# Kernel tuning notes

Measured on AMD Instinct MI355X. Metric: run time of the kernel, lower is better.

Reference implementation:

```python
import jax, jax.numpy as jnp
import numpy as np

B, S, D = 2, 2048, 2048
H, KVH = 16, 4
HD = D // H  # 128


def _rope_angles(seq, head_dim):
    theta = 1.0 / (10000.0 ** (jnp.arange(0, head_dim, 2, dtype=jnp.float32) / head_dim))
    ang = jnp.arange(seq, dtype=jnp.float32)[:, None] * theta[None, :]  # [S, HD/2]
    return jnp.cos(ang), jnp.sin(ang)


def _apply_rotary(t, cos, sin):
    # t: [B, S, h, HD]; pairs are (even, odd) along last dim (view_as_complex semantics)
    tr = t[..., 0::2]
    ti = t[..., 1::2]
    c = cos[None, :, None, :]
    s = sin[None, :, None, :]
    out_r = tr * c - ti * s
    out_i = tr * s + ti * c
    return jnp.stack([out_r, out_i], axis=-1).reshape(t.shape)


def setup_inputs() -> dict:
    key = jax.random.key(0)
    ks = jax.random.split(key, 8)
    sd = 1.0 / np.sqrt(D)
    return {
        'x': jax.random.normal(ks[0], (B, S, D), dtype=jnp.float32),
        'wq': jax.random.normal(ks[1], (D, D), dtype=jnp.float32) * sd,
        'bq': jax.random.normal(ks[2], (D,), dtype=jnp.float32) * 0.01,
        'wk': jax.random.normal(ks[3], (D, KVH * HD), dtype=jnp.float32) * sd,
        'bk': jax.random.normal(ks[4], (KVH * HD,), dtype=jnp.float32) * 0.01,
        'wv': jax.random.normal(ks[5], (D, KVH * HD), dtype=jnp.float32) * sd,
        'bv': jax.random.normal(ks[6], (KVH * HD,), dtype=jnp.float32) * 0.01,
        'wo': jax.random.normal(ks[7], (D, D), dtype=jnp.float32) * sd,
    }


def reference(x, wq, bq, wk, bk, wv, bv, wo):
    b, s, d = x.shape
    q = (x @ wq + bq).reshape(b, s, H, HD)
    k = (x @ wk + bk).reshape(b, s, KVH, HD)
    v = (x @ wv + bv).reshape(b, s, KVH, HD)

    cos, sin = _rope_angles(s, HD)
    q = _apply_rotary(q, cos, sin)
    k = _apply_rotary(k, cos, sin)

    repeat = H // KVH
    k = jnp.repeat(k, repeat, axis=2)  # [B, S, H, HD]
    v = jnp.repeat(v, repeat, axis=2)

    scale = 1.0 / np.sqrt(HD)
    att_score = jnp.einsum('bqhd,bkhd->bqhk', q, k) * scale  # [B, S, H, S]
    att_weight = jax.nn.softmax(att_score, axis=-1)
    out = jnp.einsum('bqhk,bkhd->bqhd', att_weight, v)
    out = out.reshape(b, s, H * HD)
    return out @ wo
```

## Files before the change

### kernel.cpp

```cpp
#include <hip/hip_runtime.h>
#include <hip/hip_bf16.h>
#include <cstdint>

typedef __attribute__((ext_vector_type(4))) float f32x4;
typedef __attribute__((ext_vector_type(16))) float f32x16;
typedef __attribute__((ext_vector_type(8))) short bf16x8;
typedef __attribute__((ext_vector_type(4))) unsigned int u32x4;
typedef unsigned short u16;
typedef unsigned int u32;

__device__ __forceinline__ u16 f2b(float x) {
  __hip_bfloat16 h = __float2bfloat16(x);
  return *reinterpret_cast<u16*>(&h);
}

__device__ __forceinline__ float b2f(u32 u) {
  u32 v = u << 16;
  return __builtin_bit_cast(float, v);
}

__device__ __forceinline__ u32 pk(float a, float b) {
  __hip_bfloat162 h2 = __float22bfloat162_rn(float2{a, b});
  return *reinterpret_cast<u32*>(&h2);
}

__device__ __forceinline__ void gload16(const void* g, void* l) {
  __builtin_amdgcn_global_load_lds((const __attribute__((address_space(1))) u32*)g,
                                   (__attribute__((address_space(3))) u32*)l, 16, 0, 0);
}

__device__ __forceinline__ float xmax32(float x) {
  return fmaxf(x, __shfl_xor(x, 32, 64));
}
__device__ __forceinline__ float xsum32(float x) {
  return x + __shfl_xor(x, 32, 64);
}


__global__ void cvt_f32_bf16(const float* __restrict__ in, u16* __restrict__ out, int n4) {
  int idx = (blockIdx.x * 256 + threadIdx.x);
  if (idx < n4) {
    const float4 v = *(const float4*)(in + (size_t)idx * 4);
    u16* o = out + (size_t)idx * 4;
    o[0] = f2b(v.x); o[1] = f2b(v.y); o[2] = f2b(v.z); o[3] = f2b(v.w);
  }
}

__global__ void w_transpose_cvt(const float* __restrict__ w0, const float* __restrict__ w1,
                                const float* __restrict__ w2, int b0, int b1,
                                int N0, int N1, int N2,
                                u16* __restrict__ out, int K) {
  __shared__ float tile[32][33];
  int k0 = blockIdx.x * 32, n0 = blockIdx.y * 32;
  const float* src; int srcN; int c0;
  if (n0 < b0)      { src = w0; srcN = N0; c0 = n0; }
  else if (n0 < b1) { src = w1; srcN = N1; c0 = n0 - b0; }
  else              { src = w2; srcN = N2; c0 = n0 - b1; }
  int tx = threadIdx.x & 31, ty = threadIdx.x >> 5;
#pragma unroll
  for (int j = 0; j < 32; j += 8)
    tile[ty + j][tx] = src[(size_t)(k0 + ty + j) * srcN + c0 + tx];
  __syncthreads();
#pragma unroll
  for (int j = 0; j < 32; j += 8)
    out[(size_t)(n0 + ty + j) * K + k0 + tx] = f2b(tile[tx][ty + j]);
}

__global__ void pack_bias(const float* __restrict__ bq, const float* __restrict__ bk,
                          const float* __restrict__ bv, float* __restrict__ out) {
  int i = blockIdx.x * 256 + threadIdx.x;
  if (i < 3072) out[i] = (i < 2048) ? bq[i] : ((i < 2560) ? bk[i - 2048] : bv[i - 2560]);
}

__global__ void v_transpose_cvt(const u16* __restrict__ qkv, u16* __restrict__ vt) {
  __shared__ u16 tile[32][34];
  int s0 = blockIdx.x * 32;
  int d0 = blockIdx.y * 32;
  int z = blockIdx.z;
  int b = z >> 2, kvh = z & 3;
  int tx = threadIdx.x & 31, ty = threadIdx.x >> 5;
#pragma unroll
  for (int j = 0; j < 32; j += 8)
    tile[ty + j][tx] = qkv[((size_t)(b * 2048 + s0 + ty + j)) * 3072 + 2560 + kvh * 128 + d0 + tx];
  __syncthreads();
#pragma unroll
  for (int j = 0; j < 32; j += 8)
    vt[((size_t)z * 128 + d0 + ty + j) * 2048 + s0 + tx] = tile[tx][ty + j];
}

__global__ void rope_cvt(const u16* __restrict__ qkv, u16* __restrict__ out,
                         int lognh, int col0, float scale) {
  int idx = blockIdx.x * 256 + threadIdx.x;
  int i = idx & 63;
  int nh = 1 << lognh;
  int h = (idx >> 6) & (nh - 1);
  int bs = idx >> (6 + lognh);
  int s = bs & 2047;
  int b = bs >> 11;
  u32 pr = *(const u32*)(qkv + (size_t)bs * 3072 + col0 + h * 128 + 2 * i);
  float tr = b2f(pr & 0xffffu), ti = b2f(pr >> 16);
  float theta = expf(-(float)i * 0.14391156831212787f);
  float ang = (float)s * theta;
  float sv, cv;
  sincosf(ang, &sv, &cv);
  float orr = (tr * cv - ti * sv) * scale;
  float oii = (tr * sv + ti * cv) * scale;
  *(u32*)(out + (((size_t)(b * nh + h) * 2048 + s) * 128 + 2 * i)) = pk(orr, oii);
}

__global__ __launch_bounds__(512, 2) void gemm256_bt(
    const u16* __restrict__ A, const u16* __restrict__ Bt,
    const float* __restrict__ bias, void* __restrict__ Cv,
    int M, int N, int K, int gx, int obf16) {
  __shared__ u16 lds[65536];
  const int tid = threadIdx.x, lane = tid & 63;
  const int w = tid >> 6, wr = w >> 2, wc = w & 3;
  const int nb = gridDim.x;
  const int swz = (blockIdx.x & 7) * (nb >> 3) + (blockIdx.x >> 3);
  const int m0 = (swz / gx) * 256, n0 = (swz % gx) * 256;
  const int l15 = lane & 15;
  const int gx16 = ((lane >> 4) * 16) ^ (((l15 >> 1) & 3) << 4);

#define GL(X, kh, bufi, t)                                                      \
  { _Pragma("unroll")                                                           \
    for (int rd = 0; rd < 2; ++rd) {                                            \
      int c = tid + rd * 512;                                                   \
      int row = c >> 2;                                                         \
      int sx = ((c & 3) * 16) ^ (((row >> 1) & 3) << 4);                        \
      const u16* srcp = ((X) ? Bt + (size_t)(n0 + row) * K                      \
                             : A + (size_t)(m0 + row) * K) + (t) * 64 + (kh) * 32; \
      gload16((const char*)srcp + sx,                                           \
              (char*)lds + (bufi) * 65536 + (X) * 32768 + (kh) * 16384 + c * 16); \
    } }

  f32x4 acc[8][4] = {};
  const int NT = K >> 6;

  GL(0, 0, 0, 0) GL(1, 0, 0, 0) GL(0, 1, 0, 0) GL(1, 1, 0, 0)

  for (int t = 0; t < NT; ++t) {
    const int buf = t & 1, nbuf = buf ^ 1;
    const int tn = (t + 1 < NT) ? t + 1 : NT - 1;
    const char* Ab = (const char*)lds + buf * 65536;
    const char* Bb = Ab + 32768;
    bf16x8 af[4], bfr[4];

    asm volatile("s_waitcnt vmcnt(4)" ::: "memory");
    __builtin_amdgcn_s_barrier();
    GL(0, 0, nbuf, tn)
#pragma unroll
    for (int n = 0; n < 4; ++n)
      bfr[n] = *(const bf16x8*)(Bb + (wc * 64 + n * 16 + l15) * 64 + gx16);
#pragma unroll
    for (int m = 0; m < 4; ++m)
      af[m] = *(const bf16x8*)(Ab + (wr * 128 + m * 16 + l15) * 64 + gx16);
    __builtin_amdgcn_s_setprio(1);
#pragma unroll
    for (int m = 0; m < 4; ++m)
#pragma unroll
      for (int n = 0; n < 4; ++n)
        acc[m][n] = __builtin_amdgcn_mfma_f32_16x16x32_bf16(af[m], bfr[n], acc[m][n], 0, 0, 0);
    __builtin_amdgcn_s_setprio(0);

    GL(1, 0, nbuf, tn)
#pragma unroll
    for (int m = 0; m < 4; ++m)
      af[m] = *(const bf16x8*)(Ab + (wr * 128 + (m + 4) * 16 + l15) * 64 + gx16);
    __builtin_amdgcn_s_setprio(1);
#pragma unroll
    for (int m = 0; m < 4; ++m)
#pragma unroll
      for (int n = 0; n < 4; ++n)
        acc[m + 4][n] = __builtin_amdgcn_mfma_f32_16x16x32_bf16(af[m], bfr[n], acc[m + 4][n], 0, 0, 0);
    __builtin_amdgcn_s_setprio(0);

    asm volatile("s_waitcnt vmcnt(4)" ::: "memory");
    __builtin_amdgcn_s_barrier();
    GL(0, 1, nbuf, tn)
#pragma unroll
    for (int n = 0; n < 4; ++n)
      bfr[n] = *(const bf16x8*)(Bb + 16384 + (wc * 64 + n * 16 + l15) * 64 + gx16);
#pragma unroll
    for (int m = 0; m < 4; ++m)
      af[m] = *(const bf16x8*)(Ab + 16384 + (wr * 128 + m * 16 + l15) * 64 + gx16);
    __builtin_amdgcn_s_setprio(1);
#pragma unroll
    for (int m = 0; m < 4; ++m)
#pragma unroll
      for (int n = 0; n < 4; ++n)
        acc[m][n] = __builtin_amdgcn_mfma_f32_16x16x32_bf16(af[m], bfr[n], acc[m][n], 0, 0, 0);
    __builtin_amdgcn_s_setprio(0);

    GL(1, 1, nbuf, tn)
#pragma unroll
    for (int m = 0; m < 4; ++m)
      af[m] = *(const bf16x8*)(Ab + 16384 + (wr * 128 + (m + 4) * 16 + l15) * 64 + gx16);
    __builtin_amdgcn_s_setprio(1);
#pragma unroll
    for (int m = 0; m < 4; ++m)
#pragma unroll
      for (int n = 0; n < 4; ++n)
        acc[m + 4][n] = __builtin_amdgcn_mfma_f32_16x16x32_bf16(af[m], bfr[n], acc[m + 4][n], 0, 0, 0);
    __builtin_amdgcn_s_setprio(0);
  }
  asm volatile("s_waitcnt vmcnt(0)" ::: "memory");

#pragma unroll
  for (int m = 0; m < 8; ++m) {
    int row = m0 + wr * 128 + m * 16 + ((lane >> 4) << 2);
#pragma unroll
    for (int n = 0; n < 4; ++n) {
      int col = n0 + wc * 64 + n * 16 + l15;
      float bvv = bias ? bias[col] : 0.f;
      if (obf16) {
        u16* cp = (u16*)Cv + (size_t)row * N + col;
#pragma unroll
        for (int r = 0; r < 4; ++r) cp[(size_t)r * N] = f2b(acc[m][n][r] + bvv);
      } else {
        float* cp = (float*)Cv + (size_t)row * N + col;
#pragma unroll
        for (int r = 0; r < 4; ++r) cp[(size_t)r * N] = acc[m][n][r] + bvv;
      }
    }
  }
}

__global__ __launch_bounds__(256) void gemm_bt_bf16(
    const u16* __restrict__ A, const u16* __restrict__ Bt,
    const float* __restrict__ bias, void* __restrict__ Cv,
    int M, int N, int K, int gx, int obf16) {
  __shared__ u16 As[128 * 32];
  __shared__ u16 Bs[128 * 32];
  const int tid = threadIdx.x;
  const int lane = tid & 63;
  const int w = tid >> 6;
  const int wr = w >> 1, wc = w & 1;
  const int nb = gridDim.x;
  const int swz = (blockIdx.x & 7) * (nb >> 3) + (blockIdx.x >> 3);
  const int m0 = (swz / gx) * 128;
  const int n0 = (swz % gx) * 128;

  f32x4 acc[4][4] = {};

  for (int k0 = 0; k0 < K; k0 += 32) {
#pragma unroll
    for (int it = 0; it < 2; ++it) {
      int c = tid + it * 256;
      int row = c >> 2;
      int off = (c & 3) * 8;
      gload16(A + (size_t)(m0 + row) * K + k0 + off, (u16*)As + w * 512 + it * 2048);
      gload16(Bt + (size_t)(n0 + row) * K + k0 + off, (u16*)Bs + w * 512 + it * 2048);
    }
    __syncthreads();
    const int col8 = (lane >> 4) * 8;
    bf16x8 a[4], bfr[4];
#pragma unroll
    for (int m = 0; m < 4; ++m)
      a[m] = *(const bf16x8*)&As[(wr * 64 + m * 16 + (lane & 15)) * 32 + col8];
#pragma unroll
    for (int n = 0; n < 4; ++n)
      bfr[n] = *(const bf16x8*)&Bs[(wc * 64 + n * 16 + (lane & 15)) * 32 + col8];
#pragma unroll
    for (int m = 0; m < 4; ++m)
#pragma unroll
      for (int n = 0; n < 4; ++n)
        acc[m][n] = __builtin_amdgcn_mfma_f32_16x16x32_bf16(a[m], bfr[n], acc[m][n], 0, 0, 0);
    __syncthreads();
  }

#pragma unroll
  for (int m = 0; m < 4; ++m) {
    int row = m0 + wr * 64 + m * 16 + ((lane >> 4) << 2);
#pragma unroll
    for (int n = 0; n < 4; ++n) {
      int col = n0 + wc * 64 + n * 16 + (lane & 15);
      float bvv = bias ? bias[col] : 0.f;
      if (obf16) {
        u16* cp = (u16*)Cv + (size_t)row * N + col;
#pragma unroll
        for (int r = 0; r < 4; ++r) cp[(size_t)r * N] = f2b(acc[m][n][r] + bvv);
      } else {
        float* cp = (float*)Cv + (size_t)row * N + col;
#pragma unroll
        for (int r = 0; r < 4; ++r) cp[(size_t)r * N] = acc[m][n][r] + bvv;
      }
    }
  }
}

__global__ __launch_bounds__(128, 3) void flash_attn(
    const u16* __restrict__ Qr, const u16* __restrict__ Kr,
    const u16* __restrict__ Vt, u16* __restrict__ Att) {
  __shared__ u16 Ks[2][32 * 128];
  __shared__ u16 Vs[2][128 * 32];
  const int tid = threadIdx.x, lane = tid & 63, w = tid >> 6;
  const int lo = lane & 31, hi = lane >> 5;
  const int q0 = blockIdx.x * 64 + w * 32;
  const int h = blockIdx.y, b = blockIdx.z;
  const int kvh = h >> 2;

  const char* Khead = (const char*)(Kr + (size_t)(b * 4 + kvh) * 2048 * 128);
  const char* Vhead = (const char*)(Vt + (size_t)(b * 4 + kvh) * 128 * 2048);

  bf16x8 qf[8];
  {
    const u16* qp = Qr + ((size_t)(b * 16 + h) * 2048 + q0 + lo) * 128 + hi * 8;
#pragma unroll
    for (int ds = 0; ds < 8; ++ds) qf[ds] = *(const bf16x8*)(qp + ds * 16);
  }

#define STAGE(bufi, t)                                                        \
  {                                                                           \
    _Pragma("unroll")                                                         \
    for (int it = 0; it < 4; ++it) {                                          \
      int c = it * 128 + tid;                                                 \
      int krow = c >> 4;                                                      \
      int koff = krow * 256 + ((c & 15) << 4 ^ ((krow & 7) << 4));            \
      gload16(Khead + (size_t)(t) * 8192 + koff,                              \
              (u16*)Ks[bufi] + it * 1024 + w * 512);                          \
      int vrow = c >> 2;                                                      \
      int voff = vrow * 4096 + ((c & 3) << 4 ^ (((vrow >> 1) & 3) << 4));     \
      gload16(Vhead + (size_t)(t) * 64 + voff,                                \
              (u16*)Vs[bufi] + it * 1024 + w * 512);                          \
    }                                                                         \
  }

  f32x16 o0 = {}, o1 = {}, o2 = {}, o3 = {};
  float m_run = -3.0e38f, l_run = 0.f;
  const int swz = (lo & 7) << 4;
  const int vswz = ((lo >> 1) & 3) << 4;
  const int hi16 = hi * 16;

  STAGE(0, 0);
  __syncthreads();

  int buf = 0;
  for (int t = 0; t < 64; ++t) {
    int tn = (t < 63) ? t + 1 : 63;
    STAGE(buf ^ 1, tn);

    const char* Kb = (const char*)Ks[buf];
    const char* Vb = (const char*)Vs[buf];

    f32x16 sc = {};
    __builtin_amdgcn_s_setprio(1);
#pragma unroll
    for (int ds = 0; ds < 8; ++ds) {
      bf16x8 kf = *(const bf16x8*)(Kb + lo * 256 + ((ds * 32 + hi16) ^ swz));
      sc = __builtin_amdgcn_mfma_f32_32x32x16_bf16(kf, qf[ds], sc, 0, 0, 0);
    }
    __builtin_amdgcn_s_setprio(0);

    float m01 = fmaxf(fmaxf(sc[0], sc[1]), fmaxf(sc[2], sc[3]));
    float m23 = fmaxf(fmaxf(sc[4], sc[5]), fmaxf(sc[6], sc[7]));
    float m45 = fmaxf(fmaxf(sc[8], sc[9]), fmaxf(sc[10], sc[11]));
    float m67 = fmaxf(fmaxf(sc[12], sc[13]), fmaxf(sc[14], sc[15]));
    float pmax = xmax32(fmaxf(fmaxf(m01, m23), fmaxf(m45, m67)));

    if (!__all(pmax - m_run <= 8.0f)) {
      float mnew = fmaxf(m_run, pmax);
      float rs = __expf(m_run - mnew);
      m_run = mnew;
      l_run *= rs;
#pragma unroll
      for (int r = 0; r < 16; ++r) {
        float rsr = __shfl(rs, (r & 3) + 8 * (r >> 2) + 4 * hi, 64);
        o0[r] *= rsr; o1[r] *= rsr; o2[r] *= rsr; o3[r] *= rsr;
      }
    }

    float lsum = 0.f;
#pragma unroll
    for (int r = 0; r < 16; ++r) { float p = __expf(sc[r] - m_run); sc[r] = p; lsum += p; }
    l_run += xsum32(lsum);

    bf16x8 pa0, pa1;
    {
      u32 a0 = pk(sc[0], sc[1]),   a1 = pk(sc[2], sc[3]);
      u32 b0 = pk(sc[4], sc[5]),   b1 = pk(sc[6], sc[7]);
      u32 t0 = hi ? a0 : b0, t1 = hi ? a1 : b1;
      u32 r0 = __shfl_xor(t0, 32, 64), r1 = __shfl_xor(t1, 32, 64);
      u32x4 w0;
      w0[0] = hi ? r0 : a0; w0[1] = hi ? r1 : a1;
      w0[2] = hi ? b0 : r0; w0[3] = hi ? b1 : r1;
      pa0 = __builtin_bit_cast(bf16x8, w0);
      u32 c0 = pk(sc[8], sc[9]),   c1 = pk(sc[10], sc[11]);
      u32 d0 = pk(sc[12], sc[13]), d1 = pk(sc[14], sc[15]);
      u32 t2 = hi ? c0 : d0, t3 = hi ? c1 : d1;
      u32 r2 = __shfl_xor(t2, 32, 64), r3 = __shfl_xor(t3, 32, 64);
      u32x4 w1;
      w1[0] = hi ? r2 : c0; w1[1] = hi ? r3 : c1;
      w1[2] = hi ? d0 : r2; w1[3] = hi ? d1 : r3;
      pa1 = __builtin_bit_cast(bf16x8, w1);
    }

    __builtin_amdgcn_s_setprio(1);
#define PVN(on, n)                                                                                     \
    {                                                                                                  \
      const char* vrb = Vb + ((n) * 32 + lo) * 64;                                                     \
      on = __builtin_amdgcn_mfma_f32_32x32x16_bf16(pa0, *(const bf16x8*)(vrb + ((0  + hi16) ^ vswz)), on, 0, 0, 0); \
      on = __builtin_amdgcn_mfma_f32_32x32x16_bf16(pa1, *(const bf16x8*)(vrb + ((32 + hi16) ^ vswz)), on, 0, 0, 0); \
    }
    PVN(o0, 0)
    PVN(o1, 1)
    PVN(o2, 2)
    PVN(o3, 3)
    __builtin_amdgcn_s_setprio(0);

    __syncthreads();
    buf ^= 1;
  }

  float inv = 1.0f / l_run;
  size_t rowbase = (size_t)(b * 2048 + q0);
#pragma unroll
  for (int r = 0; r < 16; ++r) {
    int rr = (r & 3) + 8 * (r >> 2) + 4 * hi;
    float invr = __shfl(inv, rr, 64);
    u16* op = Att + (rowbase + rr) * 2048 + h * 128 + lo;
    op[0]  = f2b(o0[r] * invr);
    op[32] = f2b(o1[r] * invr);
    op[64] = f2b(o2[r] * invr);
    op[96] = f2b(o3[r] * invr);
  }
}


extern "C" void kernel_launch(void* const* d_in, const int* in_sizes, int n_in,
                              void* d_out, int out_size, void* d_ws, size_t ws_size,
                              hipStream_t stream) {
  const float* x  = (const float*)d_in[0];
  const float* wq = (const float*)d_in[1];
  const float* bq = (const float*)d_in[2];
  const float* wk = (const float*)d_in[3];
  const float* bk = (const float*)d_in[4];
  const float* wv = (const float*)d_in[5];
  const float* bv = (const float*)d_in[6];
  const float* wo = (const float*)d_in[7];
  float* out = (float*)d_out;
  char* ws = (char*)d_ws;

  u16*   x_bf   = (u16*)  (ws + 0);
  u16*   att    = (u16*)  (ws + 0);
  u16*   wqkv_t = (u16*)  (ws + 16777216);
  u16*   wo_t   = (u16*)  (ws + 29360128);
  float* biasq  = (float*)(ws + 37748736);
  u16*   qkv    = (u16*)  (ws + 37761024);
  u16*   q_r    = (u16*)  (ws + 88092672);
  u16*   k_r    = (u16*)  (ws + 104869888);
  u16*   v_t    = (u16*)  (ws + 109064192);

  cvt_f32_bf16<<<8192, 256, 0, stream>>>(x, x_bf, 2097152);
  w_transpose_cvt<<<dim3(64, 96), 256, 0, stream>>>(wq, wk, wv, 2048, 2560,
                                                    2048, 512, 512, wqkv_t, 2048);
  w_transpose_cvt<<<dim3(64, 64), 256, 0, stream>>>(wo, wo, wo, 2048, 2560,
                                                    2048, 2048, 2048, wo_t, 2048);
  pack_bias<<<12, 256, 0, stream>>>(bq, bk, bv, biasq);

  gemm256_bt<<<192, 512, 0, stream>>>(x_bf, wqkv_t, biasq, qkv, 4096, 3072, 2048, 12, 1);

  rope_cvt<<<16384, 256, 0, stream>>>(qkv, q_r, 4, 0, 0.08838834764831845f);
  rope_cvt<<<4096, 256, 0, stream>>>(qkv, k_r, 2, 2048, 1.0f);
  v_transpose_cvt<<<dim3(64, 4, 8), 256, 0, stream>>>(qkv, v_t);

  flash_attn<<<dim3(32, 16, 2), 128, 0, stream>>>(q_r, k_r, v_t, att);

  gemm_bt_bf16<<<512, 256, 0, stream>>>(att, wo_t, nullptr, out, 4096, 2048, 2048, 16, 0);
}
```

Baseline: 278.2 us.

## Replace output-projection GEMM with pipelined 128x256 kernel and merge prep launches

The output projection GEMM moves from a simple 128x128 tile kernel, which synchronises twice per 32-wide K step, to a 128x256 tile kernel with 8 waves. The new kernel double-buffers 64-wide K tiles in LDS with swizzled addressing, interleaves the next tile's global loads with the MFMAs, and raises wave priority around the MFMA block. The two weight-transpose launches become one kernel, and the bias-pack kernel is removed by reading the separate bias arrays directly in the QKV GEMM epilogue. This cuts launch overhead and should improve the compute efficiency of the output GEMM, but the larger tile gives only 256 blocks, which may leave some CUs underused.

```diff
diff --git a/kernel.cpp b/kernel.cpp
--- a/kernel.cpp
+++ b/kernel.cpp
@@ -46,16 +46,21 @@
   }
 }
 
-__global__ void w_transpose_cvt(const float* __restrict__ w0, const float* __restrict__ w1,
-                                const float* __restrict__ w2, int b0, int b1,
-                                int N0, int N1, int N2,
-                                u16* __restrict__ out, int K) {
+__global__ void w_transpose_all(const float* __restrict__ wq, const float* __restrict__ wk,
+                                const float* __restrict__ wv, const float* __restrict__ wo,
+                                u16* __restrict__ wqkv_t, u16* __restrict__ wo_t) {
   __shared__ float tile[32][33];
-  int k0 = blockIdx.x * 32, n0 = blockIdx.y * 32;
-  const float* src; int srcN; int c0;
-  if (n0 < b0)      { src = w0; srcN = N0; c0 = n0; }
-  else if (n0 < b1) { src = w1; srcN = N1; c0 = n0 - b0; }
-  else              { src = w2; srcN = N2; c0 = n0 - b1; }
+  int k0 = blockIdx.x * 32;
+  int by = blockIdx.y;
+  const float* src; int srcN; int c0; u16* out; int n0;
+  if (by < 96) {
+    n0 = by * 32; out = wqkv_t;
+    if (n0 < 2048)      { src = wq; srcN = 2048; c0 = n0; }
+    else if (n0 < 2560) { src = wk; srcN = 512;  c0 = n0 - 2048; }
+    else                { src = wv; srcN = 512;  c0 = n0 - 2560; }
+  } else {
+    n0 = (by - 96) * 32; out = wo_t; src = wo; srcN = 2048; c0 = n0;
+  }
   int tx = threadIdx.x & 31, ty = threadIdx.x >> 5;
 #pragma unroll
   for (int j = 0; j < 32; j += 8)
@@ -63,13 +68,7 @@
   __syncthreads();
 #pragma unroll
   for (int j = 0; j < 32; j += 8)
-    out[(size_t)(n0 + ty + j) * K + k0 + tx] = f2b(tile[tx][ty + j]);
-}
-
-__global__ void pack_bias(const float* __restrict__ bq, const float* __restrict__ bk,
-                          const float* __restrict__ bv, float* __restrict__ out) {
-  int i = blockIdx.x * 256 + threadIdx.x;
-  if (i < 3072) out[i] = (i < 2048) ? bq[i] : ((i < 2560) ? bk[i - 2048] : bv[i - 2560]);
+    out[(size_t)(n0 + ty + j) * 2048 + k0 + tx] = f2b(tile[tx][ty + j]);
 }
 
 __global__ void v_transpose_cvt(const u16* __restrict__ qkv, u16* __restrict__ vt) {
@@ -110,8 +109,9 @@
 
 __global__ __launch_bounds__(512, 2) void gemm256_bt(
     const u16* __restrict__ A, const u16* __restrict__ Bt,
-    const float* __restrict__ bias, void* __restrict__ Cv,
-    int M, int N, int K, int gx, int obf16) {
+    const float* __restrict__ bq, const float* __restrict__ bk,
+    const float* __restrict__ bv, u16* __restrict__ C,
+    int M, int N, int K, int gx) {
   __shared__ u16 lds[65536];
   const int tid = threadIdx.x, lane = tid & 63;
   const int w = tid >> 6, wr = w >> 2, wc = w & 3;
@@ -211,79 +211,88 @@
 #pragma unroll
     for (int n = 0; n < 4; ++n) {
       int col = n0 + wc * 64 + n * 16 + l15;
-      float bvv = bias ? bias[col] : 0.f;
-      if (obf16) {
-        u16* cp = (u16*)Cv + (size_t)row * N + col;
-#pragma unroll
-        for (int r = 0; r < 4; ++r) cp[(size_t)r * N] = f2b(acc[m][n][r] + bvv);
-      } else {
-        float* cp = (float*)Cv + (size_t)row * N + col;
-#pragma unroll
-        for (int r = 0; r < 4; ++r) cp[(size_t)r * N] = acc[m][n][r] + bvv;
-      }
-    }
-  }
-}
-
-__global__ __launch_bounds__(256) void gemm_bt_bf16(
+      float bvv = (col < 2048) ? bq[col] : ((col < 2560) ? bk[col - 2048] : bv[col - 2560]);
+      u16* cp = C + (size_t)row * N + col;
+#pragma unroll
+      for (int r = 0; r < 4; ++r) cp[(size_t)r * N] = f2b(acc[m][n][r] + bvv);
+    }
+  }
+}
+
+__global__ __launch_bounds__(512, 1) void gemm128x256_bt(
     const u16* __restrict__ A, const u16* __restrict__ Bt,
-    const float* __restrict__ bias, void* __restrict__ Cv,
-    int M, int N, int K, int gx, int obf16) {
-  __shared__ u16 As[128 * 32];
-  __shared__ u16 Bs[128 * 32];
-  const int tid = threadIdx.x;
-  const int lane = tid & 63;
-  const int w = tid >> 6;
-  const int wr = w >> 1, wc = w & 1;
+    float* __restrict__ C, int M, int N, int K, int gx) {
+  __shared__ u16 lds[49152];
+  const int tid = threadIdx.x, lane = tid & 63;
+  const int w = tid >> 6, wr = w >> 2, wc = w & 3;
   const int nb = gridDim.x;
   const int swz = (blockIdx.x & 7) * (nb >> 3) + (blockIdx.x >> 3);
-  const int m0 = (swz / gx) * 128;
-  const int n0 = (swz % gx) * 128;
+  const int m0 = (swz / gx) * 128, n0 = (swz % gx) * 256;
+  const int l15 = lane & 15;
+  const int gx16 = ((lane >> 4) * 16) ^ (((l15 >> 1) & 3) << 4);
+
+#define GLA(kh, bufi, t)                                                        \
+  { int c = tid;                                                                \
+    int row = c >> 2;                                                           \
+    int sx = ((c & 3) * 16) ^ (((row >> 1) & 3) << 4);                          \
+    const u16* srcp = A + (size_t)(m0 + row) * K + (t) * 64 + (kh) * 32;        \
+    gload16((const char*)srcp + sx,                                             \
+            (char*)lds + (bufi) * 16384 + (kh) * 8192 + c * 16); }
+
+#define GLB(kh, bufi, t)                                                        \
+  { _Pragma("unroll")                                                           \
+    for (int rd = 0; rd < 2; ++rd) {                                            \
+      int c = tid + rd * 512;                                                   \
+      int row = c >> 2;                                                         \
+      int sx = ((c & 3) * 16) ^ (((row >> 1) & 3) << 4);                        \
+      const u16* srcp = Bt + (size_t)(n0 + row) * K + (t) * 64 + (kh) * 32;     \
+      gload16((const char*)srcp + sx,                                           \
+              (char*)lds + 32768 + (bufi) * 32768 + (kh) * 16384 + c * 16); } }
 
   f32x4 acc[4][4] = {};
-
-  for (int k0 = 0; k0 < K; k0 += 32) {
-#pragma unroll
-    for (int it = 0; it < 2; ++it) {
-      int c = tid + it * 256;
-      int row = c >> 2;
-      int off = (c & 3) * 8;
-      gload16(A + (size_t)(m0 + row) * K + k0 + off, (u16*)As + w * 512 + it * 2048);
-      gload16(Bt + (size_t)(n0 + row) * K + k0 + off, (u16*)Bs + w * 512 + it * 2048);
-    }
-    __syncthreads();
-    const int col8 = (lane >> 4) * 8;
-    bf16x8 a[4], bfr[4];
-#pragma unroll
-    for (int m = 0; m < 4; ++m)
-      a[m] = *(const bf16x8*)&As[(wr * 64 + m * 16 + (lane & 15)) * 32 + col8];
-#pragma unroll
-    for (int n = 0; n < 4; ++n)
-      bfr[n] = *(const bf16x8*)&Bs[(wc * 64 + n * 16 + (lane & 15)) * 32 + col8];
-#pragma unroll
-    for (int m = 0; m < 4; ++m)
+  const int NT = K >> 6;
+
+  GLA(0, 0, 0) GLB(0, 0, 0) GLA(1, 0, 0) GLB(1, 0, 0)
+
+  for (int t = 0; t < NT; ++t) {
+    const int buf = t & 1, nbuf = buf ^ 1;
+    const int tn = (t + 1 < NT) ? t + 1 : NT - 1;
+    const char* Ab = (const char*)lds + buf * 16384;
+    const char* Bb = (const char*)lds + 32768 + buf * 32768;
+    bf16x8 af[4], bfr[4];
+
+#pragma unroll
+    for (int kh = 0; kh < 2; ++kh) {
+      asm volatile("s_waitcnt vmcnt(3)" ::: "memory");
+      __builtin_amdgcn_s_barrier();
+      if (kh == 0) { GLA(0, nbuf, tn) GLB(0, nbuf, tn) }
+      else         { GLA(1, nbuf, tn) GLB(1, nbuf, tn) }
 #pragma unroll
       for (int n = 0; n < 4; ++n)
-        acc[m][n] = __builtin_amdgcn_mfma_f32_16x16x32_bf16(a[m], bfr[n], acc[m][n], 0, 0, 0);
-    __syncthreads();
-  }
+        bfr[n] = *(const bf16x8*)(Bb + kh * 16384 + (wc * 64 + n * 16 + l15) * 64 + gx16);
+#pragma unroll
+      for (int m = 0; m < 4; ++m)
+        af[m] = *(const bf16x8*)(Ab + kh * 8192 + (wr * 64 + m * 16 + l15) * 64 + gx16);
+      __builtin_amdgcn_s_setprio(1);
+#pragma unroll
+      for (int m = 0; m < 4; ++m)
+#pragma unroll
+        for (int n = 0; n < 4; ++n)
+          acc[m][n] = __builtin_amdgcn_mfma_f32_16x16x32_bf16(af[m], bfr[n], acc[m][n], 0, 0, 0);
+      __builtin_amdgcn_s_setprio(0);
+    }
+  }
+  asm volatile("s_waitcnt vmcnt(0)" ::: "memory");
 
 #pragma unroll
   for (int m = 0; m < 4; ++m) {
     int row = m0 + wr * 64 + m * 16 + ((lane >> 4) << 2);
 #pragma unroll
     for (int n = 0; n < 4; ++n) {
-      int col = n0 + wc * 64 + n * 16 + (lane & 15);
-      float bvv = bias ? bias[col] : 0.f;
-      if (obf16) {
-        u16* cp = (u16*)Cv + (size_t)row * N + col;
-#pragma unroll
-        for (int r = 0; r < 4; ++r) cp[(size_t)r * N] = f2b(acc[m][n][r] + bvv);
-      } else {
-        float* cp = (float*)Cv + (size_t)row * N + col;
-#pragma unroll
-        for (int r = 0; r < 4; ++r) cp[(size_t)r * N] = acc[m][n][r] + bvv;
-      }
+      int col = n0 + wc * 64 + n * 16 + l15;
+      float* cp = C + (size_t)row * N + col;
+#pragma unroll
+      for (int r = 0; r < 4; ++r) cp[(size_t)r * N] = acc[m][n][r];
     }
   }
 }
@@ -444,20 +453,15 @@
   u16*   att    = (u16*)  (ws + 0);
   u16*   wqkv_t = (u16*)  (ws + 16777216);
   u16*   wo_t   = (u16*)  (ws + 29360128);
-  float* biasq  = (float*)(ws + 37748736);
   u16*   qkv    = (u16*)  (ws + 37761024);
   u16*   q_r    = (u16*)  (ws + 88092672);
   u16*   k_r    = (u16*)  (ws + 104869888);
   u16*   v_t    = (u16*)  (ws + 109064192);
 
   cvt_f32_bf16<<<8192, 256, 0, stream>>>(x, x_bf, 2097152);
-  w_transpose_cvt<<<dim3(64, 96), 256, 0, stream>>>(wq, wk, wv, 2048, 2560,
-                                                    2048, 512, 512, wqkv_t, 2048);
-  w_transpose_cvt<<<dim3(64, 64), 256, 0, stream>>>(wo, wo, wo, 2048, 2560,
-                                                    2048, 2048, 2048, wo_t, 2048);
-  pack_bias<<<12, 256, 0, stream>>>(bq, bk, bv, biasq);
-
-  gemm256_bt<<<192, 512, 0, stream>>>(x_bf, wqkv_t, biasq, qkv, 4096, 3072, 2048, 12, 1);
+  w_transpose_all<<<dim3(64, 160), 256, 0, stream>>>(wq, wk, wv, wo, wqkv_t, wo_t);
+
+  gemm256_bt<<<192, 512, 0, stream>>>(x_bf, wqkv_t, bq, bk, bv, qkv, 4096, 3072, 2048, 12);
 
   rope_cvt<<<16384, 256, 0, stream>>>(qkv, q_r, 4, 0, 0.08838834764831845f);
   rope_cvt<<<4096, 256, 0, stream>>>(qkv, k_r, 2, 2048, 1.0f);
@@ -465,5 +469,5 @@
 
   flash_attn<<<dim3(32, 16, 2), 128, 0, stream>>>(q_r, k_r, v_t, att);
 
-  gemm_bt_bf16<<<512, 256, 0, stream>>>(att, wo_t, nullptr, out, 4096, 2048, 2048, 16, 0);
-}
+  gemm128x256_bt<<<256, 512, 0, stream>>>(att, wo_t, out, 4096, 2048, 2048, 8);
+}
```

After: 256.6 us. -7.8%, faster.
